# Performance work log

Measured on AMD Instinct MI355X. Metric: run time of the kernel, lower is better.

## Reference

```python
import jax, jax.numpy as jnp
import numpy as np

B, T, E, H = 2, 1024, 1024, 16
D = E // H  # per-head dim = 64; softmax scale uses sqrt(D) per SelfAttentionHead.embedding_dim
SCALE = float(np.sqrt(D))


def setup_inputs() -> dict:
    key = jax.random.key(0)
    ks = jax.random.split(key, 10)
    s = 1.0 / np.sqrt(D)
    sf = 1.0 / np.sqrt(E)
    return {
        "x": jax.random.normal(ks[0], (B, T, E), dtype=jnp.float32),
        # per-head linear params, stacked over head index i: (H, D, D) / (H, D)
        "Wq": jax.random.uniform(ks[1], (H, D, D), minval=-s, maxval=s, dtype=jnp.float32),
        "bq": jax.random.uniform(ks[2], (H, D), minval=-s, maxval=s, dtype=jnp.float32),
        "Wk": jax.random.uniform(ks[3], (H, D, D), minval=-s, maxval=s, dtype=jnp.float32),
        "bk": jax.random.uniform(ks[4], (H, D), minval=-s, maxval=s, dtype=jnp.float32),
        "Wv": jax.random.uniform(ks[5], (H, D, D), minval=-s, maxval=s, dtype=jnp.float32),
        "bv": jax.random.uniform(ks[6], (H, D), minval=-s, maxval=s, dtype=jnp.float32),
        "Wf": jax.random.uniform(ks[7], (E, E), minval=-sf, maxval=sf, dtype=jnp.float32),
        "bf": jax.random.uniform(ks[8], (E,), minval=-sf, maxval=sf, dtype=jnp.float32),
    }


def reference(x, Wq, bq, Wk, bk, Wv, bv, Wf, bf):
    # (B, T, E) -> (B, H, T, D)
    xh = x.reshape(B, T, H, D).transpose(0, 2, 1, 3)
    # each head i applies its own D->D linears to the FULL (B,H,T,D) tensor
    # q/k/v: (B, H, T, I, D) where I indexes the head (param set)
    q = jnp.einsum('bhtd,ied->bhtie', xh, Wq) + bq
    k = jnp.einsum('bhtd,ied->bhtie', xh, Wk) + bk
    v = jnp.einsum('bhtd,ied->bhtie', xh, Wv) + bv
    # attention over the FEATURE dimension: scores are (B,H,I,D,D)
    scores = jnp.einsum('bhtip,bhtiq->bhipq', q, k) / SCALE
    w = jax.nn.softmax(scores, axis=-1)
    # (B,H,I,D,D) x (B,H,T,I,D) -> (B,H,T,I,D)
    o = jnp.einsum('bhipq,bhtiq->bhtip', w, v)
    # concat head outputs along last dim: (B,H,T,I*D) = (B,H,T,E)
    cat = o.reshape(B, H, T, E)
    # final Linear(E,E)
    return jnp.einsum('bhte,fe->bhtf', cat, Wf) + bf
```

## Files before the change

### kernel.cpp

```cpp
#include <hip/hip_runtime.h>

#define TT 1024
#define EE 1024

typedef __attribute__((ext_vector_type(8))) short short8;
typedef __attribute__((ext_vector_type(4))) float floatx4;
typedef __attribute__((ext_vector_type(4))) unsigned short ushort4v;
typedef __attribute__((ext_vector_type(8))) unsigned short ushort8v;

static __device__ __forceinline__ unsigned short f2bf(float f) {
  union { float f; unsigned int u; } v; v.f = f;
  unsigned int u = v.u;
  u += 0x7FFFu + ((u >> 16) & 1u);
  return (unsigned short)(u >> 16);
}
static __device__ __forceinline__ float bf2f(unsigned short u) {
  union { unsigned int i; float f; } v; v.i = ((unsigned int)u) << 16;
  return v.f;
}
static __device__ __forceinline__ void splitbf(float x, unsigned short& h,
                                               unsigned short& l) {
  h = f2bf(x);
  l = f2bf(x - bf2f(h));
}
static __device__ __forceinline__ unsigned short* lp(const unsigned short* t,
                                                     int row, int byte) {
  return (unsigned short*)((const char*)t + row * 128 + (byte ^ ((row & 7) << 4)));
}
static __device__ __forceinline__ short8 ldf(const unsigned short* t, int row,
                                             int byte) {
  return *(const short8*)((const char*)t + row * 128 + (byte ^ ((row & 7) << 4)));
}

__global__ __launch_bounds__(256) void kP(const float* __restrict__ x,
                                          const float* __restrict__ Wf,
                                          float* __restrict__ Sxx_part,
                                          float* __restrict__ sx_part,
                                          unsigned short* __restrict__ Wfbf,
                                          unsigned short* __restrict__ xbf) {
  const int bx = blockIdx.x;
  const int r = threadIdx.x;
  if (bx >= 256) {
    const int wb = bx - 256;
#pragma unroll
    for (int it = 0; it < 4; ++it) {
      int idx = wb * 4096 + it * 1024 + r * 4;
      float4 v = *reinterpret_cast<const float4*>(&Wf[idx]);
      ushort4v o;
      o[0] = f2bf(v.x); o[1] = f2bf(v.y); o[2] = f2bf(v.z); o[3] = f2bf(v.w);
      *reinterpret_cast<ushort4v*>(&Wfbf[idx]) = o;
    }
    return;
  }
  const int bh = bx >> 3, chunk = bx & 7;
  const int b = bh >> 4, h = bh & 15;
  const int t0 = chunk * 128;
  __shared__ float Xs[128 * 64];
  const float* xb = x + ((size_t)b * TT + t0) * EE + h * 64;
#pragma unroll
  for (int j = 0; j < 8; ++j) {
    int idx4 = j * 256 + r;
    int t = idx4 >> 4, c4 = idx4 & 15;
    *reinterpret_cast<float4*>(&Xs[t * 64 + c4 * 4]) =
        *reinterpret_cast<const float4*>(&xb[(size_t)t * EE + c4 * 4]);
  }
  __syncthreads();
#pragma unroll
  for (int j = 0; j < 4; ++j) {
    int idx8 = j * 256 + r;
    int t = idx8 >> 3, gch = idx8 & 7;
    ushort8v o;
#pragma unroll
    for (int e = 0; e < 8; ++e) o[e] = f2bf(Xs[t * 64 + gch * 8 + e]);
    *reinterpret_cast<ushort8v*>(&xbf[((size_t)bh * TT + t0 + t) * 64 + gch * 8]) = o;
  }
  const int p0 = (r >> 4) * 4, q0 = (r & 15) * 4;
  float acc[4][4] = {};
  for (int t = 0; t < 128; ++t) {
    float4 pv = *reinterpret_cast<const float4*>(&Xs[t * 64 + p0]);
    float4 qv = *reinterpret_cast<const float4*>(&Xs[t * 64 + q0]);
    float pa[4] = {pv.x, pv.y, pv.z, pv.w};
    float qa[4] = {qv.x, qv.y, qv.z, qv.w};
#pragma unroll
    for (int i = 0; i < 4; ++i)
#pragma unroll
      for (int j = 0; j < 4; ++j) acc[i][j] += pa[i] * qa[j];
  }
  float* Sb = Sxx_part + ((size_t)chunk * 32 + bh) * 4096;
#pragma unroll
  for (int i = 0; i < 4; ++i) {
    float4 v = make_float4(acc[i][0], acc[i][1], acc[i][2], acc[i][3]);
    *reinterpret_cast<float4*>(&Sb[(p0 + i) * 64 + q0]) = v;
  }
  if (r < 64) {
    float s = 0.f;
    for (int t = 0; t < 128; ++t) s += Xs[t * 64 + r];
    sx_part[(chunk * 32 + bh) * 64 + r] = s;
  }
}

__global__ __launch_bounds__(256) void kB1(const float* __restrict__ Sxx_part,
                                           const float* __restrict__ sx_part,
                                           const float* __restrict__ Wq,
                                           const float* __restrict__ bq,
                                           const float* __restrict__ Wk,
                                           const float* __restrict__ bk,
                                           const float* __restrict__ Wv,
                                           const float* __restrict__ bv,
                                           unsigned short* __restrict__ Mtbf) {
  const int blk = blockIdx.x;
  const int bh = blk & 31, ih = blk >> 5;
  const int r = threadIdx.x;
  const int w = r >> 6, l = r & 63;
  const int wm = w >> 1, wn = w & 1;
  const int lm = l & 15, lk = l >> 4;

  __shared__ unsigned short TSh[4096], TSl[4096];
  __shared__ unsigned short TWh[4096], TWl[4096];
  __shared__ unsigned short TAh[4096], TAl[4096];
  __shared__ float SC[64 * 68];
  __shared__ float svec[64], qsv[64], ksv[64], bqv[64], bkv[64], bvv[64];

#pragma unroll
  for (int it = 0; it < 4; ++it) {
    int idx = it * 1024 + r * 4;
    int row = idx >> 6, c0 = idx & 63;
    float4 vs = *(const float4*)&Sxx_part[(size_t)bh * 4096 + idx];
#pragma unroll
    for (int ch = 1; ch < 8; ++ch) {
      float4 tv = *(const float4*)&Sxx_part[((size_t)ch * 32 + bh) * 4096 + idx];
      vs.x += tv.x; vs.y += tv.y; vs.z += tv.z; vs.w += tv.w;
    }
    float4 vw = *(const float4*)&Wq[ih * 4096 + idx];
    float fs[4] = {vs.x, vs.y, vs.z, vs.w};
    float fw[4] = {vw.x, vw.y, vw.z, vw.w};
    ushort4v sh, sl, wh, wl;
#pragma unroll
    for (int j = 0; j < 4; ++j) {
      unsigned short th, tl;
      splitbf(fs[j], th, tl);
      sh[j] = th; sl[j] = tl;
      splitbf(fw[j], th, tl);
      wh[j] = th; wl[j] = tl;
    }
    *(ushort4v*)lp(TSh, row, c0 * 2) = sh;
    *(ushort4v*)lp(TSl, row, c0 * 2) = sl;
    *(ushort4v*)lp(TWh, row, c0 * 2) = wh;
    *(ushort4v*)lp(TWl, row, c0 * 2) = wl;
  }
  if (r < 64) {
    float s = 0.f;
#pragma unroll
    for (int ch = 0; ch < 8; ++ch) s += sx_part[(ch * 32 + bh) * 64 + r];
    svec[r] = s;
    bqv[r] = bq[ih * 64 + r];
    bkv[r] = bk[ih * 64 + r];
    bvv[r] = bv[ih * 64 + r];
  }
  __syncthreads();

  floatx4 a1[2][2] = {};
  {
    short8 Ah[2][2], Al[2][2], Bh[2][2], Bl[2][2];
#pragma unroll
    for (int mt = 0; mt < 2; ++mt)
#pragma unroll
      for (int ks = 0; ks < 2; ++ks) {
        Ah[mt][ks] = ldf(TWh, wm * 32 + mt * 16 + lm, ks * 64 + lk * 16);
        Al[mt][ks] = ldf(TWl, wm * 32 + mt * 16 + lm, ks * 64 + lk * 16);
        Bh[mt][ks] = ldf(TSh, wn * 32 + mt * 16 + lm, ks * 64 + lk * 16);
        Bl[mt][ks] = ldf(TSl, wn * 32 + mt * 16 + lm, ks * 64 + lk * 16);
      }
#pragma unroll
    for (int ks = 0; ks < 2; ++ks)
#pragma unroll
      for (int mt = 0; mt < 2; ++mt)
#pragma unroll
        for (int nt = 0; nt < 2; ++nt) {
          a1[mt][nt] = __builtin_amdgcn_mfma_f32_16x16x32_bf16(Ah[mt][ks], Bh[nt][ks], a1[mt][nt], 0, 0, 0);
          a1[mt][nt] = __builtin_amdgcn_mfma_f32_16x16x32_bf16(Ah[mt][ks], Bl[nt][ks], a1[mt][nt], 0, 0, 0);
          a1[mt][nt] = __builtin_amdgcn_mfma_f32_16x16x32_bf16(Al[mt][ks], Bh[nt][ks], a1[mt][nt], 0, 0, 0);
        }
  }
#pragma unroll
  for (int mt = 0; mt < 2; ++mt)
#pragma unroll
    for (int nt = 0; nt < 2; ++nt)
#pragma unroll
      for (int q = 0; q < 4; ++q) {
        int p = wm * 32 + mt * 16 + lk * 4 + q;
        int dd = wn * 32 + nt * 16 + lm;
        unsigned short h, lo2;
        splitbf(a1[mt][nt][q], h, lo2);
        *lp(TAh, p, dd * 2) = h;
        *lp(TAl, p, dd * 2) = lo2;
      }
  {
    int p = r >> 2, dc = (r & 3) * 16;
    float s = 0.f;
#pragma unroll
    for (int j = 0; j < 16; ++j) {
      int d = dc + j;
      s += (bf2f(*lp(TWh, p, d * 2)) + bf2f(*lp(TWl, p, d * 2))) * svec[d];
    }
    s += __shfl_xor(s, 1);
    s += __shfl_xor(s, 2);
    if ((r & 3) == 0) qsv[p] = s;
  }
  __syncthreads();

#pragma unroll
  for (int it = 0; it < 4; ++it) {
    int idx = it * 1024 + r * 4;
    int row = idx >> 6, c0 = idx & 63;
    float4 vw = *(const float4*)&Wk[ih * 4096 + idx];
    float fw[4] = {vw.x, vw.y, vw.z, vw.w};
    ushort4v wh, wl;
#pragma unroll
    for (int j = 0; j < 4; ++j) {
      unsigned short th, tl;
      splitbf(fw[j], th, tl);
      wh[j] = th; wl[j] = tl;
    }
    *(ushort4v*)lp(TWh, row, c0 * 2) = wh;
    *(ushort4v*)lp(TWl, row, c0 * 2) = wl;
    float4 vv = *(const float4*)&Wv[ih * 4096 + idx];
    int q = row, d0 = c0;
    *lp(TSh, d0 + 0, q * 2) = f2bf(vv.x);
    *lp(TSh, d0 + 1, q * 2) = f2bf(vv.y);
    *lp(TSh, d0 + 2, q * 2) = f2bf(vv.z);
    *lp(TSh, d0 + 3, q * 2) = f2bf(vv.w);
  }
  __syncthreads();
  {
    int p = r >> 2, dc = (r & 3) * 16;
    float s = 0.f;
#pragma unroll
    for (int j = 0; j < 16; ++j) {
      int d = dc + j;
      s += (bf2f(*lp(TWh, p, d * 2)) + bf2f(*lp(TWl, p, d * 2))) * svec[d];
    }
    s += __shfl_xor(s, 1);
    s += __shfl_xor(s, 2);
    if ((r & 3) == 0) ksv[p] = s;
  }
  floatx4 a2[2][2] = {};
  {
    short8 Ah[2][2], Al[2][2], Bh[2][2], Bl[2][2];
#pragma unroll
    for (int mt = 0; mt < 2; ++mt)
#pragma unroll
      for (int ks = 0; ks < 2; ++ks) {
        Ah[mt][ks] = ldf(TAh, wm * 32 + mt * 16 + lm, ks * 64 + lk * 16);
        Al[mt][ks] = ldf(TAl, wm * 32 + mt * 16 + lm, ks * 64 + lk * 16);
        Bh[mt][ks] = ldf(TWh, wn * 32 + mt * 16 + lm, ks * 64 + lk * 16);
        Bl[mt][ks] = ldf(TWl, wn * 32 + mt * 16 + lm, ks * 64 + lk * 16);
      }
#pragma unroll
    for (int ks = 0; ks < 2; ++ks)
#pragma unroll
      for (int mt = 0; mt < 2; ++mt)
#pragma unroll
        for (int nt = 0; nt < 2; ++nt) {
          a2[mt][nt] = __builtin_amdgcn_mfma_f32_16x16x32_bf16(Ah[mt][ks], Bh[nt][ks], a2[mt][nt], 0, 0, 0);
          a2[mt][nt] = __builtin_amdgcn_mfma_f32_16x16x32_bf16(Ah[mt][ks], Bl[nt][ks], a2[mt][nt], 0, 0, 0);
          a2[mt][nt] = __builtin_amdgcn_mfma_f32_16x16x32_bf16(Al[mt][ks], Bh[nt][ks], a2[mt][nt], 0, 0, 0);
        }
  }
  __syncthreads();
#pragma unroll
  for (int mt = 0; mt < 2; ++mt)
#pragma unroll
    for (int nt = 0; nt < 2; ++nt)
#pragma unroll
      for (int q = 0; q < 4; ++q) {
        int p = wm * 32 + mt * 16 + lk * 4 + q;
        int qq = wn * 32 + nt * 16 + lm;
        float v = a2[mt][nt][q] + qsv[p] * bkv[qq] + bqv[p] * ksv[qq] +
                  1024.f * bqv[p] * bkv[qq];
        SC[p * 68 + qq] = v * 0.125f;
      }
  __syncthreads();
  {
    int p = r >> 2, qc = (r & 3) * 16;
    float e[16];
    float m = -1e30f;
#pragma unroll
    for (int j = 0; j < 16; ++j) {
      e[j] = SC[p * 68 + qc + j];
      m = fmaxf(m, e[j]);
    }
    m = fmaxf(m, __shfl_xor(m, 1));
    m = fmaxf(m, __shfl_xor(m, 2));
    float s = 0.f, cp = 0.f;
#pragma unroll
    for (int j = 0; j < 16; ++j) {
      float ex = __expf(e[j] - m);
      e[j] = ex;
      s += ex;
      cp += ex * bvv[qc + j];
    }
    s += __shfl_xor(s, 1);
    s += __shfl_xor(s, 2);
    cp += __shfl_xor(cp, 1);
    cp += __shfl_xor(cp, 2);
    float inv = 1.f / s;
#pragma unroll
    for (int j = 0; j < 16; ++j) *lp(TSl, p, (qc + j) * 2) = f2bf(e[j] * inv);
    if ((r & 3) == 0)
      Mtbf[(size_t)(2048 + bh) * 1024 + ih * 64 + p] = f2bf(cp * inv);
  }
  __syncthreads();
  floatx4 a3[2][2] = {};
  {
    short8 A3[2][2], B3[2][2];
#pragma unroll
    for (int mt = 0; mt < 2; ++mt)
#pragma unroll
      for (int ks = 0; ks < 2; ++ks) {
        A3[mt][ks] = ldf(TSh, wm * 32 + mt * 16 + lm, ks * 64 + lk * 16);
        B3[mt][ks] = ldf(TSl, wn * 32 + mt * 16 + lm, ks * 64 + lk * 16);
      }
#pragma unroll
    for (int ks = 0; ks < 2; ++ks)
#pragma unroll
      for (int mt = 0; mt < 2; ++mt)
#pragma unroll
        for (int nt = 0; nt < 2; ++nt)
          a3[mt][nt] = __builtin_amdgcn_mfma_f32_16x16x32_bf16(A3[mt][ks], B3[nt][ks], a3[mt][nt], 0, 0, 0);
  }
#pragma unroll
  for (int mt = 0; mt < 2; ++mt)
#pragma unroll
    for (int nt = 0; nt < 2; ++nt)
#pragma unroll
      for (int q = 0; q < 4; ++q) {
        int d = wm * 32 + mt * 16 + lk * 4 + q;
        int p = wn * 32 + nt * 16 + lm;
        Mtbf[(size_t)(bh * 64 + d) * 1024 + ih * 64 + p] = f2bf(a3[mt][nt][q]);
      }
}

__global__ __launch_bounds__(256) void kC(const unsigned short* __restrict__ xbf,
                                          const unsigned short* __restrict__ Wfbf,
                                          const unsigned short* __restrict__ Mtbf,
                                          const float* __restrict__ bfv,
                                          float* __restrict__ out) {
  const int fx = blockIdx.x, bh = blockIdx.y;
  const int f0 = fx * 128;
  const int r = threadIdx.x;
  const int w = r >> 6, l = r & 63;
  const int lm = l & 15, lk = l >> 4;

  __shared__ __align__(16) unsigned short GT[128 * 64];
  __shared__ __align__(16) unsigned short cL[1024];
  __shared__ float gL[128];

  if (r < 128)
    *reinterpret_cast<ushort8v*>(&cL[r * 8]) = *reinterpret_cast<const ushort8v*>(
        &Mtbf[(size_t)(2048 + bh) * 1024 + r * 8]);
  __syncthreads();

  {
    const int wf = w >> 1, wd = w & 1;
    const unsigned short* ap = Wfbf + (size_t)(f0 + wf * 64 + lm) * 1024 + lk * 8;
    const unsigned short* bp = Mtbf + (size_t)(bh * 64 + wd * 32 + lm) * 1024 + lk * 8;
    floatx4 acc[4][2] = {};
    floatx4 gacc[4] = {};
    for (int k0 = 0; k0 < 1024; k0 += 64) {
      short8 a[4][2], b[2][2], cf[2];
#pragma unroll
      for (int mi = 0; mi < 4; ++mi)
#pragma unroll
        for (int ks = 0; ks < 2; ++ks)
          a[mi][ks] = *reinterpret_cast<const short8*>(ap + mi * 16 * 1024 + k0 + ks * 32);
#pragma unroll
      for (int ni = 0; ni < 2; ++ni)
#pragma unroll
        for (int ks = 0; ks < 2; ++ks)
          b[ni][ks] = *reinterpret_cast<const short8*>(bp + ni * 16 * 1024 + k0 + ks * 32);
#pragma unroll
      for (int ks = 0; ks < 2; ++ks)
        cf[ks] = *reinterpret_cast<const short8*>(&cL[k0 + ks * 32 + lk * 8]);
#pragma unroll
      for (int ks = 0; ks < 2; ++ks)
#pragma unroll
        for (int mi = 0; mi < 4; ++mi) {
#pragma unroll
          for (int ni = 0; ni < 2; ++ni)
            acc[mi][ni] = __builtin_amdgcn_mfma_f32_16x16x32_bf16(
                a[mi][ks], b[ni][ks], acc[mi][ni], 0, 0, 0);
          if (wd == 0)
            gacc[mi] = __builtin_amdgcn_mfma_f32_16x16x32_bf16(
                a[mi][ks], cf[ks], gacc[mi], 0, 0, 0);
        }
    }
#pragma unroll
    for (int mi = 0; mi < 4; ++mi)
#pragma unroll
      for (int ni = 0; ni < 2; ++ni)
#pragma unroll
        for (int q = 0; q < 4; ++q) {
          int fl = wf * 64 + mi * 16 + lk * 4 + q;
          int d = wd * 32 + ni * 16 + lm;
          *lp(GT, fl, d * 2) = f2bf(acc[mi][ni][q]);
        }
    if (wd == 0 && lm == 0) {
#pragma unroll
      for (int mi = 0; mi < 4; ++mi)
#pragma unroll
        for (int q = 0; q < 4; ++q) {
          int fl = wf * 64 + mi * 16 + lk * 4 + q;
          gL[fl] = gacc[mi][q] + bfv[f0 + fl];
        }
    }
  }
  __syncthreads();

  const int wt = w >> 1, wc = w & 1;
  float gv[4];
#pragma unroll
  for (int ni = 0; ni < 4; ++ni) gv[ni] = gL[wc * 64 + ni * 16 + lm];
  short8 bfr[4][2];
#pragma unroll
  for (int ni = 0; ni < 4; ++ni)
#pragma unroll
    for (int ks = 0; ks < 2; ++ks)
      bfr[ni][ks] = ldf(GT, wc * 64 + ni * 16 + lm, (ks * 32 + lk * 8) * 2);
  float* ob = out + (size_t)bh * 1048576;
  for (int t0 = 0; t0 < 1024; t0 += 128) {
    const unsigned short* ap =
        xbf + (size_t)bh * 65536 + (size_t)(t0 + wt * 64 + lm) * 64 + lk * 8;
    short8 a[4][2];
#pragma unroll
    for (int mi = 0; mi < 4; ++mi)
#pragma unroll
      for (int ks = 0; ks < 2; ++ks)
        a[mi][ks] = *reinterpret_cast<const short8*>(ap + mi * 16 * 64 + ks * 32);
    floatx4 acc[4][4] = {};
#pragma unroll
    for (int ks = 0; ks < 2; ++ks)
#pragma unroll
      for (int mi = 0; mi < 4; ++mi)
#pragma unroll
        for (int ni = 0; ni < 4; ++ni)
          acc[mi][ni] = __builtin_amdgcn_mfma_f32_16x16x32_bf16(
              a[mi][ks], bfr[ni][ks], acc[mi][ni], 0, 0, 0);
#pragma unroll
    for (int mi = 0; mi < 4; ++mi)
#pragma unroll
      for (int ni = 0; ni < 4; ++ni) {
        const int f = f0 + wc * 64 + ni * 16 + lm;
#pragma unroll
        for (int q = 0; q < 4; ++q) {
          const int t = t0 + wt * 64 + mi * 16 + lk * 4 + q;
          ob[(size_t)t * 1024 + f] = acc[mi][ni][q] + gv[ni];
        }
      }
  }
}

extern "C" void kernel_launch(void* const* d_in, const int* in_sizes, int n_in,
                              void* d_out, int out_size, void* d_ws, size_t ws_size,
                              hipStream_t stream) {
  const float* x = (const float*)d_in[0];
  const float* Wq = (const float*)d_in[1];
  const float* bq = (const float*)d_in[2];
  const float* Wk = (const float*)d_in[3];
  const float* bk = (const float*)d_in[4];
  const float* Wv = (const float*)d_in[5];
  const float* bv = (const float*)d_in[6];
  const float* Wf = (const float*)d_in[7];
  const float* bf = (const float*)d_in[8];
  float* out = (float*)d_out;

  float* ws = (float*)d_ws;
  float* Sxx_part = ws;
  float* sx_part = Sxx_part + 1048576;
  unsigned short* Wfbf = (unsigned short*)(sx_part + 16384);
  unsigned short* xbf = Wfbf + 1048576;
  unsigned short* Mtbf = xbf + 2097152;

  kP<<<512, 256, 0, stream>>>(x, Wf, Sxx_part, sx_part, Wfbf, xbf);
  kB1<<<512, 256, 0, stream>>>(Sxx_part, sx_part, Wq, bq, Wk, bk, Wv, bv, Mtbf);
  kC<<<dim3(8, 32), 256, 0, stream>>>(xbf, Wfbf, Mtbf, bf, out);
}
```

Baseline: 79.80 us.

## Fuse Gram-matrix precompute into kB1 and convert Wf to bf16 inside kC

Removes the separate kP kernel. Each kB1 block now streams its head's x slice, computes the x^T x Gram matrix and column sums with split-bf16 MFMA, and writes xbf when ih==0. kC now loads fp32 Wf and converts it to bf16 on the fly instead of reading a pre-converted copy. This saves one launch and the workspace round trips, but every kB1 block recomputes the same Gram matrix 16 times and kC reads twice the bytes for Wf.

```diff
diff --git a/kernel.cpp b/kernel.cpp
--- a/kernel.cpp
+++ b/kernel.cpp
@@ -31,85 +31,29 @@
                                              int byte) {
   return *(const short8*)((const char*)t + row * 128 + (byte ^ ((row & 7) << 4)));
 }
-
-__global__ __launch_bounds__(256) void kP(const float* __restrict__ x,
-                                          const float* __restrict__ Wf,
-                                          float* __restrict__ Sxx_part,
-                                          float* __restrict__ sx_part,
-                                          unsigned short* __restrict__ Wfbf,
-                                          unsigned short* __restrict__ xbf) {
-  const int bx = blockIdx.x;
-  const int r = threadIdx.x;
-  if (bx >= 256) {
-    const int wb = bx - 256;
-#pragma unroll
-    for (int it = 0; it < 4; ++it) {
-      int idx = wb * 4096 + it * 1024 + r * 4;
-      float4 v = *reinterpret_cast<const float4*>(&Wf[idx]);
-      ushort4v o;
-      o[0] = f2bf(v.x); o[1] = f2bf(v.y); o[2] = f2bf(v.z); o[3] = f2bf(v.w);
-      *reinterpret_cast<ushort4v*>(&Wfbf[idx]) = o;
-    }
-    return;
-  }
-  const int bh = bx >> 3, chunk = bx & 7;
-  const int b = bh >> 4, h = bh & 15;
-  const int t0 = chunk * 128;
-  __shared__ float Xs[128 * 64];
-  const float* xb = x + ((size_t)b * TT + t0) * EE + h * 64;
-#pragma unroll
-  for (int j = 0; j < 8; ++j) {
-    int idx4 = j * 256 + r;
-    int t = idx4 >> 4, c4 = idx4 & 15;
-    *reinterpret_cast<float4*>(&Xs[t * 64 + c4 * 4]) =
-        *reinterpret_cast<const float4*>(&xb[(size_t)t * EE + c4 * 4]);
-  }
-  __syncthreads();
-#pragma unroll
-  for (int j = 0; j < 4; ++j) {
-    int idx8 = j * 256 + r;
-    int t = idx8 >> 3, gch = idx8 & 7;
-    ushort8v o;
-#pragma unroll
-    for (int e = 0; e < 8; ++e) o[e] = f2bf(Xs[t * 64 + gch * 8 + e]);
-    *reinterpret_cast<ushort8v*>(&xbf[((size_t)bh * TT + t0 + t) * 64 + gch * 8]) = o;
-  }
-  const int p0 = (r >> 4) * 4, q0 = (r & 15) * 4;
-  float acc[4][4] = {};
-  for (int t = 0; t < 128; ++t) {
-    float4 pv = *reinterpret_cast<const float4*>(&Xs[t * 64 + p0]);
-    float4 qv = *reinterpret_cast<const float4*>(&Xs[t * 64 + q0]);
-    float pa[4] = {pv.x, pv.y, pv.z, pv.w};
-    float qa[4] = {qv.x, qv.y, qv.z, qv.w};
-#pragma unroll
-    for (int i = 0; i < 4; ++i)
-#pragma unroll
-      for (int j = 0; j < 4; ++j) acc[i][j] += pa[i] * qa[j];
-  }
-  float* Sb = Sxx_part + ((size_t)chunk * 32 + bh) * 4096;
-#pragma unroll
-  for (int i = 0; i < 4; ++i) {
-    float4 v = make_float4(acc[i][0], acc[i][1], acc[i][2], acc[i][3]);
-    *reinterpret_cast<float4*>(&Sb[(p0 + i) * 64 + q0]) = v;
-  }
-  if (r < 64) {
-    float s = 0.f;
-    for (int t = 0; t < 128; ++t) s += Xs[t * 64 + r];
-    sx_part[(chunk * 32 + bh) * 64 + r] = s;
-  }
-}
-
-__global__ __launch_bounds__(256) void kB1(const float* __restrict__ Sxx_part,
-                                           const float* __restrict__ sx_part,
+static __device__ __forceinline__ short8 ldwf(const float* p) {
+  float4 a = *reinterpret_cast<const float4*>(p);
+  float4 b = *reinterpret_cast<const float4*>(p + 4);
+  ushort8v o;
+  o[0] = f2bf(a.x); o[1] = f2bf(a.y); o[2] = f2bf(a.z); o[3] = f2bf(a.w);
+  o[4] = f2bf(b.x); o[5] = f2bf(b.y); o[6] = f2bf(b.z); o[7] = f2bf(b.w);
+  union { ushort8v u; short8 s; } cv;
+  cv.u = o;
+  return cv.s;
+}
+
+__global__ __launch_bounds__(256) void kB1(const float* __restrict__ x,
                                            const float* __restrict__ Wq,
                                            const float* __restrict__ bq,
                                            const float* __restrict__ Wk,
                                            const float* __restrict__ bk,
                                            const float* __restrict__ Wv,
                                            const float* __restrict__ bv,
-                                           unsigned short* __restrict__ Mtbf) {
+                                           unsigned short* __restrict__ Mtbf,
+                                           unsigned short* __restrict__ xbf) {
   const int blk = blockIdx.x;
   const int bh = blk & 31, ih = blk >> 5;
+  const int b = bh >> 4, h = bh & 15;
   const int r = threadIdx.x;
   const int w = r >> 6, l = r & 63;
   const int wm = w >> 1, wn = w & 1;
@@ -119,39 +63,97 @@
   __shared__ unsigned short TWh[4096], TWl[4096];
   __shared__ unsigned short TAh[4096], TAl[4096];
   __shared__ float SC[64 * 68];
+  __shared__ float sxp[1024];
   __shared__ float svec[64], qsv[64], ksv[64], bqv[64], bkv[64], bvv[64];
 
+#pragma unroll
+  for (int j = 0; j < 4; ++j) sxp[j * 256 + r] = 0.f;
+  __syncthreads();
+
+  const int tg = r >> 4;
+  const int d0s = (r & 15) * 4;
+  floatx4 sacc[2][2] = {};
+  const float* xb = x + (size_t)b * TT * EE + h * 64;
+  for (int c = 0; c < 16; ++c) {
+#pragma unroll
+    for (int it = 0; it < 4; ++it) {
+      int tl = it * 16 + tg;
+      float4 v = *reinterpret_cast<const float4*>(
+          &xb[(size_t)(c * 64 + tl) * EE + d0s]);
+      float fv[4] = {v.x, v.y, v.z, v.w};
+      unsigned short hi[4];
+#pragma unroll
+      for (int j = 0; j < 4; ++j) {
+        unsigned short th, tlo;
+        splitbf(fv[j], th, tlo);
+        hi[j] = th;
+        *lp(TSh, d0s + j, tl * 2) = th;
+        *lp(TSl, d0s + j, tl * 2) = tlo;
+        sxp[tg * 64 + d0s + j] += fv[j];
+      }
+      if (ih == 0) {
+        ushort4v o;
+        o[0] = hi[0]; o[1] = hi[1]; o[2] = hi[2]; o[3] = hi[3];
+        *reinterpret_cast<ushort4v*>(
+            &xbf[((size_t)bh * TT + c * 64 + tl) * 64 + d0s]) = o;
+      }
+    }
+    __syncthreads();
+    short8 Ah[2][2], Al[2][2], Bh[2][2], Bl[2][2];
+#pragma unroll
+    for (int mt = 0; mt < 2; ++mt)
+#pragma unroll
+      for (int ks = 0; ks < 2; ++ks) {
+        Ah[mt][ks] = ldf(TSh, wm * 32 + mt * 16 + lm, ks * 64 + lk * 16);
+        Al[mt][ks] = ldf(TSl, wm * 32 + mt * 16 + lm, ks * 64 + lk * 16);
+        Bh[mt][ks] = ldf(TSh, wn * 32 + mt * 16 + lm, ks * 64 + lk * 16);
+        Bl[mt][ks] = ldf(TSl, wn * 32 + mt * 16 + lm, ks * 64 + lk * 16);
+      }
+#pragma unroll
+    for (int ks = 0; ks < 2; ++ks)
+#pragma unroll
+      for (int mt = 0; mt < 2; ++mt)
+#pragma unroll
+        for (int nt = 0; nt < 2; ++nt) {
+          sacc[mt][nt] = __builtin_amdgcn_mfma_f32_16x16x32_bf16(Ah[mt][ks], Bh[nt][ks], sacc[mt][nt], 0, 0, 0);
+          sacc[mt][nt] = __builtin_amdgcn_mfma_f32_16x16x32_bf16(Ah[mt][ks], Bl[nt][ks], sacc[mt][nt], 0, 0, 0);
+          sacc[mt][nt] = __builtin_amdgcn_mfma_f32_16x16x32_bf16(Al[mt][ks], Bh[nt][ks], sacc[mt][nt], 0, 0, 0);
+        }
+    __syncthreads();
+  }
+#pragma unroll
+  for (int mt = 0; mt < 2; ++mt)
+#pragma unroll
+    for (int nt = 0; nt < 2; ++nt)
+#pragma unroll
+      for (int q = 0; q < 4; ++q) {
+        int p = wm * 32 + mt * 16 + lk * 4 + q;
+        int dd = wn * 32 + nt * 16 + lm;
+        unsigned short h2, l2;
+        splitbf(sacc[mt][nt][q], h2, l2);
+        *lp(TSh, p, dd * 2) = h2;
+        *lp(TSl, p, dd * 2) = l2;
+      }
 #pragma unroll
   for (int it = 0; it < 4; ++it) {
     int idx = it * 1024 + r * 4;
     int row = idx >> 6, c0 = idx & 63;
-    float4 vs = *(const float4*)&Sxx_part[(size_t)bh * 4096 + idx];
-#pragma unroll
-    for (int ch = 1; ch < 8; ++ch) {
-      float4 tv = *(const float4*)&Sxx_part[((size_t)ch * 32 + bh) * 4096 + idx];
-      vs.x += tv.x; vs.y += tv.y; vs.z += tv.z; vs.w += tv.w;
-    }
     float4 vw = *(const float4*)&Wq[ih * 4096 + idx];
-    float fs[4] = {vs.x, vs.y, vs.z, vs.w};
     float fw[4] = {vw.x, vw.y, vw.z, vw.w};
-    ushort4v sh, sl, wh, wl;
+    ushort4v wh, wl;
 #pragma unroll
     for (int j = 0; j < 4; ++j) {
-      unsigned short th, tl;
-      splitbf(fs[j], th, tl);
-      sh[j] = th; sl[j] = tl;
-      splitbf(fw[j], th, tl);
-      wh[j] = th; wl[j] = tl;
-    }
-    *(ushort4v*)lp(TSh, row, c0 * 2) = sh;
-    *(ushort4v*)lp(TSl, row, c0 * 2) = sl;
+      unsigned short th, tl2;
+      splitbf(fw[j], th, tl2);
+      wh[j] = th; wl[j] = tl2;
+    }
     *(ushort4v*)lp(TWh, row, c0 * 2) = wh;
     *(ushort4v*)lp(TWl, row, c0 * 2) = wl;
   }
   if (r < 64) {
     float s = 0.f;
 #pragma unroll
-    for (int ch = 0; ch < 8; ++ch) s += sx_part[(ch * 32 + bh) * 64 + r];
+    for (int g = 0; g < 16; ++g) s += sxp[g * 64 + r];
     svec[r] = s;
     bqv[r] = bq[ih * 64 + r];
     bkv[r] = bk[ih * 64 + r];
@@ -190,9 +192,9 @@
       for (int q = 0; q < 4; ++q) {
         int p = wm * 32 + mt * 16 + lk * 4 + q;
         int dd = wn * 32 + nt * 16 + lm;
-        unsigned short h, lo2;
-        splitbf(a1[mt][nt][q], h, lo2);
-        *lp(TAh, p, dd * 2) = h;
+        unsigned short h2, lo2;
+        splitbf(a1[mt][nt][q], h2, lo2);
+        *lp(TAh, p, dd * 2) = h2;
         *lp(TAl, p, dd * 2) = lo2;
       }
   {
@@ -218,9 +220,9 @@
     ushort4v wh, wl;
 #pragma unroll
     for (int j = 0; j < 4; ++j) {
-      unsigned short th, tl;
-      splitbf(fw[j], th, tl);
-      wh[j] = th; wl[j] = tl;
+      unsigned short th, tl2;
+      splitbf(fw[j], th, tl2);
+      wh[j] = th; wl[j] = tl2;
     }
     *(ushort4v*)lp(TWh, row, c0 * 2) = wh;
     *(ushort4v*)lp(TWl, row, c0 * 2) = wl;
@@ -342,7 +344,7 @@
 }
 
 __global__ __launch_bounds__(256) void kC(const unsigned short* __restrict__ xbf,
-                                          const unsigned short* __restrict__ Wfbf,
+                                          const float* __restrict__ Wf,
                                           const unsigned short* __restrict__ Mtbf,
                                           const float* __restrict__ bfv,
                                           float* __restrict__ out) {
@@ -363,7 +365,7 @@
 
   {
     const int wf = w >> 1, wd = w & 1;
-    const unsigned short* ap = Wfbf + (size_t)(f0 + wf * 64 + lm) * 1024 + lk * 8;
+    const float* ap = Wf + (size_t)(f0 + wf * 64 + lm) * 1024 + lk * 8;
     const unsigned short* bp = Mtbf + (size_t)(bh * 64 + wd * 32 + lm) * 1024 + lk * 8;
     floatx4 acc[4][2] = {};
     floatx4 gacc[4] = {};
@@ -373,7 +375,7 @@
       for (int mi = 0; mi < 4; ++mi)
 #pragma unroll
         for (int ks = 0; ks < 2; ++ks)
-          a[mi][ks] = *reinterpret_cast<const short8*>(ap + mi * 16 * 1024 + k0 + ks * 32);
+          a[mi][ks] = ldwf(ap + mi * 16 * 1024 + k0 + ks * 32);
 #pragma unroll
       for (int ni = 0; ni < 2; ++ni)
 #pragma unroll
@@ -475,13 +477,9 @@
   float* out = (float*)d_out;
 
   float* ws = (float*)d_ws;
-  float* Sxx_part = ws;
-  float* sx_part = Sxx_part + 1048576;
-  unsigned short* Wfbf = (unsigned short*)(sx_part + 16384);
-  unsigned short* xbf = Wfbf + 1048576;
+  unsigned short* xbf = (unsigned short*)ws;
   unsigned short* Mtbf = xbf + 2097152;
 
-  kP<<<512, 256, 0, stream>>>(x, Wf, Sxx_part, sx_part, Wfbf, xbf);
-  kB1<<<512, 256, 0, stream>>>(Sxx_part, sx_part, Wq, bq, Wk, bk, Wv, bv, Mtbf);
-  kC<<<dim3(8, 32), 256, 0, stream>>>(xbf, Wfbf, Mtbf, bf, out);
-}
+  kB1<<<512, 256, 0, stream>>>(x, Wq, bq, Wk, bk, Wv, bv, Mtbf, xbf);
+  kC<<<dim3(8, 32), 256, 0, stream>>>(xbf, Wf, Mtbf, bf, out);
+}
```

After: 119.2 us. +49.4%, slower.
